# Performance work log

Hardware: AMD Instinct MI355X
Metric: run time of the kernel (lower is better)

The kernel has to match this reference:

```python
import jax, jax.numpy as jnp
import numpy as np

WS = (2, 7, 7)        # window_size (D, H, W)
DIM = 192
NHEADS = 6
NW = 64               # number of windows per image
BATCH = 32            # images -> B_ = NW*BATCH
CPB_HIDDEN = 512


def _make_buffers():
    # continuous relative coords table, shape (1, 2Wd-1, 2Wh-1, 2Ww-1, 3)
    axes = [np.arange(-(w - 1), w, dtype=np.float32) for w in WS]
    table = np.stack(np.meshgrid(*axes, indexing='ij'), axis=-1)[None]
    for i in range(3):
        table[..., i] /= (WS[i] - 1)
    table *= 8
    table = np.sign(table) * np.log2(np.abs(table) + 1.0) / np.log2(8)
    # relative position index, shape (N, N)
    coords = np.stack(np.meshgrid(np.arange(WS[0]), np.arange(WS[1]), np.arange(WS[2]), indexing='ij'))
    cf = coords.reshape(3, -1)
    rel = (cf[:, :, None] - cf[:, None, :]).transpose(1, 2, 0).astype(np.int64)
    rel[..., 0] += WS[0] - 1
    rel[..., 1] += WS[1] - 1
    rel[..., 2] += WS[2] - 1
    rel[..., 0] *= (2 * WS[1] - 1) * (2 * WS[2] - 1)
    rel[..., 1] *= 2 * WS[2] - 1
    rpi = rel.sum(-1)
    return jnp.asarray(table, jnp.float32), jnp.asarray(rpi, jnp.int32)


def setup_inputs() -> dict:
    key = jax.random.key(0)
    ks = jax.random.split(key, 10)
    N = WS[0] * WS[1] * WS[2]
    B_ = NW * BATCH
    x = jax.random.normal(ks[0], (B_, N, DIM), jnp.float32)
    mask = jax.random.normal(ks[1], (NW, N, N), jnp.float32)
    qkv_w = jax.random.normal(ks[2], (3 * DIM, DIM), jnp.float32) * 0.02
    qkv_b = jnp.zeros((3 * DIM,), jnp.float32)
    logit_scale = jnp.log(10.0 * jnp.ones((NHEADS, 1, 1), jnp.float32))
    cpb_w1 = jax.random.normal(ks[3], (CPB_HIDDEN, 3), jnp.float32) * 0.02
    cpb_b1 = jnp.zeros((CPB_HIDDEN,), jnp.float32)
    cpb_w2 = jax.random.normal(ks[4], (NHEADS, CPB_HIDDEN), jnp.float32) * 0.02
    proj_w = jax.random.normal(ks[5], (DIM, DIM), jnp.float32) * 0.02
    proj_b = jnp.zeros((DIM,), jnp.float32)
    rel_coords_table, rel_pos_index = _make_buffers()
    return dict(x=x, mask=mask, qkv_w=qkv_w, qkv_b=qkv_b, logit_scale=logit_scale,
                cpb_w1=cpb_w1, cpb_b1=cpb_b1, cpb_w2=cpb_w2,
                proj_w=proj_w, proj_b=proj_b,
                rel_coords_table=rel_coords_table, rel_pos_index=rel_pos_index)


def _l2norm(t, eps=1e-12):
    # F.normalize(dim=-1): x / max(||x||, eps)
    n = jnp.sqrt(jnp.sum(t * t, axis=-1, keepdims=True))
    return t / jnp.maximum(n, eps)


def reference(x, mask, qkv_w, qkv_b, logit_scale, cpb_w1, cpb_b1, cpb_w2,
              proj_w, proj_b, rel_coords_table, rel_pos_index):
    B_, N, C = x.shape
    H = logit_scale.shape[0]
    hd = C // H
    qkv = (x @ qkv_w.T + qkv_b).reshape(B_, N, 3, H, hd).transpose(2, 0, 3, 1, 4)
    q, k, v = qkv[0], qkv[1], qkv[2]          # (B_, H, N, hd)
    attn = jnp.einsum('bhnd,bhmd->bhnm', _l2norm(q), _l2norm(k))
    scale = jnp.exp(jnp.minimum(logit_scale, jnp.log(jnp.float32(100.0))))  # (H,1,1)
    attn = attn * scale
    # continuous position bias: MLP over coords table, gather, 16*sigmoid
    hidden = jax.nn.relu(rel_coords_table @ cpb_w1.T + cpb_b1)
    tbl = (hidden @ cpb_w2.T).reshape(-1, H)
    bias = tbl[rel_pos_index.reshape(-1)].reshape(N, N, H).transpose(2, 0, 1)
    attn = attn + (16.0 * jax.nn.sigmoid(bias))[None]
    nW = mask.shape[0]
    attn = attn.reshape(B_ // nW, nW, H, N, N) + mask[None, :, None]
    attn = jax.nn.softmax(attn.reshape(B_, H, N, N), axis=-1)
    out = jnp.einsum('bhnm,bhmd->bhnd', attn, v).transpose(0, 2, 1, 3).reshape(B_, N, C)
    return out @ proj_w.T + proj_b
```

## Files before the change

### kernel.cpp

```cpp
#include <hip/hip_runtime.h>
#include <hip/hip_bf16.h>
#include <hip/hip_fp16.h>

typedef __attribute__((ext_vector_type(8))) short short8;
typedef __attribute__((ext_vector_type(4))) float f32x4;
typedef __attribute__((ext_vector_type(4))) unsigned short us4;

#define MFMA16(a, b, c) __builtin_amdgcn_mfma_f32_16x16x32_bf16(a, b, c, 0, 0, 0)
#define LN100 4.605170185988091f

__device__ __forceinline__ short f2bf(float f) {
    unsigned u = __float_as_uint(f);
    unsigned r = (u + 0x7fffu + ((u >> 16) & 1u)) >> 16;
    return (short)r;
}
__device__ __forceinline__ float h2f(unsigned short u) {
    __half_raw r; r.x = u;
    return __half2float(__half(r));
}


__global__ __launch_bounds__(256) void k_wcvt(const float* qkv_w, const float* proj_w,
                                              short* wq, short* wp) {
    int i = blockIdx.x * 256 + threadIdx.x;
    if (i < 576 * 192) wq[i] = f2bf(qkv_w[i]);
    else {
        int j = i - 576 * 192;
        if (j < 192 * 192) wp[j] = f2bf(proj_w[j]);
    }
}

__global__ __launch_bounds__(64) void k_tbl(const float* tab, const float* w1, const float* b1,
                                            const float* w2, float* tbl) {
    int e = blockIdx.x;
    int t = threadIdx.x;
    float c0 = tab[e * 3 + 0], c1 = tab[e * 3 + 1], c2 = tab[e * 3 + 2];
    float acc[6] = {0.f, 0.f, 0.f, 0.f, 0.f, 0.f};
    for (int u = t; u < 512; u += 64) {
        float hv = c0 * w1[u * 3 + 0] + c1 * w1[u * 3 + 1] + c2 * w1[u * 3 + 2] + b1[u];
        hv = fmaxf(hv, 0.f);
        #pragma unroll
        for (int hh = 0; hh < 6; ++hh) acc[hh] += hv * w2[hh * 512 + u];
    }
    #pragma unroll
    for (int hh = 0; hh < 6; ++hh) {
        float v = acc[hh];
        for (int off = 32; off > 0; off >>= 1) v += __shfl_xor(v, off, 64);
        if (t == 0) tbl[e * 6 + hh] = v;
    }
}

__global__ __launch_bounds__(256) void k_bm(const float* tbl, const int* rpi, const float* mask,
                                            __half* bm) {
    int i = blockIdx.x * 256 + threadIdx.x;
    if (i >= 64 * 6 * 98 * 112) return;
    int k = i % 112;
    int q = (i / 112) % 98;
    int h = (i / (112 * 98)) % 6;
    int w = i / (112 * 98 * 6);
    float v;
    if (k < 98) {
        float t = tbl[rpi[q * 98 + k] * 6 + h];
        v = 16.f / (1.f + expf(-t)) + mask[(w * 98 + q) * 98 + k];
    } else v = -60000.f;
    bm[i] = __float2half(v);
}

__global__ __launch_bounds__(448) void k_fused(const float* x, const short* wq, const float* qkv_b,
                                               const float* lsc, const short* wp, const float* proj_b,
                                               const __half* bm, float* outp) {
    __shared__ short lds[79872];
    short* Qs = lds;
    short* Ks = lds + 21504;
    short* VT = lds + 43008;
    short* Bs = lds + 67584;

    const int tid = threadIdx.x;
    const int wv = tid >> 6;
    const int lane = tid & 63;
    const int l16 = lane & 15, q4 = lane >> 4;
    const int b = blockIdx.x;
    const int w = b & 63;
    const f32x4 zz = {0.f, 0.f, 0.f, 0.f};

    {
        short8 z = {0, 0, 0, 0, 0, 0, 0, 0};
        #pragma unroll
        for (int it = 0; it < 7; ++it) {
            int c = tid + it * 448;
            if (c < 3072) *(short8*)&VT[c * 8] = z;
        }
    }
    short8 af[6];
    {
        int arow = wv * 16 + l16; if (arow > 97) arow = 97;
        const float* xp = x + ((size_t)b * 98 + arow) * 192 + q4 * 8;
        #pragma unroll
        for (int ks = 0; ks < 6; ++ks) {
            float4 f0 = *(const float4*)(xp + ks * 32);
            float4 f1 = *(const float4*)(xp + ks * 32 + 4);
            union { int i4[4]; short8 s; } u;
            asm("v_cvt_pk_bf16_f32 %0, %1, %2" : "=v"(u.i4[0]) : "v"(f0.x), "v"(f0.y));
            asm("v_cvt_pk_bf16_f32 %0, %1, %2" : "=v"(u.i4[1]) : "v"(f0.z), "v"(f0.w));
            asm("v_cvt_pk_bf16_f32 %0, %1, %2" : "=v"(u.i4[2]) : "v"(f1.x), "v"(f1.y));
            asm("v_cvt_pk_bf16_f32 %0, %1, %2" : "=v"(u.i4[3]) : "v"(f1.z), "v"(f1.w));
            af[ks] = u.s;
        }
    }
    short8 s0, s1, s2, s3;
    {
        int c0 = tid, c1 = tid + 448, c2 = tid + 896, c3 = tid + 1344;
        s0 = *(const short8*)(wq + (c0 / 24) * 192 + (c0 % 24) * 8);
        s1 = *(const short8*)(wq + (c1 / 24) * 192 + (c1 % 24) * 8);
        s2 = *(const short8*)(wq + (c2 / 24) * 192 + (c2 % 24) * 8);
        if (c3 < 1536) s3 = *(const short8*)(wq + (c3 / 24) * 192 + (c3 % 24) * 8);
    }
    __syncthreads();
    {
        int c0 = tid, c1 = tid + 448, c2 = tid + 896, c3 = tid + 1344;
        *(short8*)&Bs[(c0 / 24) * 192 + (((c0 % 24) ^ ((c0 / 24) & 7)) << 3)] = s0;
        *(short8*)&Bs[(c1 / 24) * 192 + (((c1 % 24) ^ ((c1 / 24) & 7)) << 3)] = s1;
        *(short8*)&Bs[(c2 / 24) * 192 + (((c2 % 24) ^ ((c2 / 24) & 7)) << 3)] = s2;
        if (c3 < 1536) *(short8*)&Bs[(c3 / 24) * 192 + (((c3 % 24) ^ ((c3 / 24) & 7)) << 3)] = s3;
    }
    __syncthreads();

    const int row_w = wv * 16 + q4 * 4;
    #pragma unroll 1
    for (int nt = 0; nt < 9; ++nt) {
        if (nt < 8) {
            const short* wn = wq + (nt + 1) * 64 * 192;
            int c0 = tid, c1 = tid + 448, c2 = tid + 896, c3 = tid + 1344;
            s0 = *(const short8*)(wn + (c0 / 24) * 192 + (c0 % 24) * 8);
            s1 = *(const short8*)(wn + (c1 / 24) * 192 + (c1 % 24) * 8);
            s2 = *(const short8*)(wn + (c2 / 24) * 192 + (c2 % 24) * 8);
            if (c3 < 1536) s3 = *(const short8*)(wn + (c3 / 24) * 192 + (c3 % 24) * 8);
        }
        f32x4 acc[4] = {zz, zz, zz, zz};
        #pragma unroll
        for (int ks = 0; ks < 6; ++ks)
            #pragma unroll
            for (int cf = 0; cf < 4; ++cf) {
                short8 bf = *(const short8*)&Bs[(cf * 16 + l16) * 192 +
                                                (((ks * 4 + q4) ^ (l16 & 7)) << 3)];
                acc[cf] = MFMA16(af[ks], bf, acc[cf]);
            }
        #pragma unroll
        for (int p = 0; p < 2; ++p) {
            int slot = nt * 2 + p;
            int which = slot / 6;
            int h = slot - which * 6;
            float bia0 = qkv_b[slot * 32 + l16];
            float bia1 = qkv_b[slot * 32 + 16 + l16];
            float sc = 1.0f;
            if (which == 0) sc = __expf(fminf(lsc[h], LN100));
            #pragma unroll
            for (int i = 0; i < 4; ++i) {
                float v0 = acc[2 * p][i] + bia0;
                float v1 = acc[2 * p + 1][i] + bia1;
                if (which < 2) {
                    float ss = v0 * v0 + v1 * v1;
                    ss += __shfl_xor(ss, 1, 16);
                    ss += __shfl_xor(ss, 2, 16);
                    ss += __shfl_xor(ss, 4, 16);
                    ss += __shfl_xor(ss, 8, 16);
                    float rn = sc / fmaxf(sqrtf(ss), 1e-12f);
                    v0 *= rn; v1 *= rn;
                }
                int row = row_w + i;
                if (which == 2) {
                    int swz = (((row >> 3) ^ (l16 & 7)) << 3) + (row & 7);
                    VT[h * 4096 + l16 * 128 + swz]        = f2bf(v0);
                    VT[h * 4096 + (l16 + 16) * 128 + swz] = f2bf(v1);
                } else {
                    short* T = (which == 0) ? Qs : Ks;
                    int c0i = h * 32 + l16, c1i = c0i + 16;
                    T[row * 192 + (((c0i >> 3) ^ (row & 7)) << 3) + (c0i & 7)] = f2bf(v0);
                    T[row * 192 + (((c1i >> 3) ^ (row & 7)) << 3) + (c1i & 7)] = f2bf(v1);
                }
            }
        }
        __syncthreads();
        if (nt < 8) {
            int c0 = tid, c1 = tid + 448, c2 = tid + 896, c3 = tid + 1344;
            *(short8*)&Bs[(c0 / 24) * 192 + (((c0 % 24) ^ ((c0 / 24) & 7)) << 3)] = s0;
            *(short8*)&Bs[(c1 / 24) * 192 + (((c1 % 24) ^ ((c1 / 24) & 7)) << 3)] = s1;
            *(short8*)&Bs[(c2 / 24) * 192 + (((c2 % 24) ^ ((c2 / 24) & 7)) << 3)] = s2;
            if (c3 < 1536) *(short8*)&Bs[(c3 / 24) * 192 + (((c3 % 24) ^ ((c3 / 24) & 7)) << 3)] = s3;
            __syncthreads();
        }
    }

    const int rq = wv * 16 + l16;
    const int qc = rq < 98 ? rq : 97;
    const int srcA = ((q4 & 1) * 2) * 16 + l16;
    const int srcB = srcA + 16;
    const bool hi = (q4 & 2) != 0;

    #pragma unroll 1
    for (int h = 0; h < 6; ++h) {
        const __half* bmp = bm + (((size_t)w * 6 + h) * 98 + qc) * 112;
        us4 bh[7];
        #pragma unroll
        for (int ct = 0; ct < 7; ++ct) bh[ct] = *(const us4*)(bmp + ct * 16 + q4 * 4);
        short8 qf = *(const short8*)&Qs[rq * 192 + (((h * 4 + q4) ^ (l16 & 7)) << 3)];
        f32x4 cc[7];
        #pragma unroll
        for (int ct = 0; ct < 7; ++ct) {
            int rk = ct * 16 + l16;
            short8 kf = *(const short8*)&Ks[rk * 192 + (((h * 4 + q4) ^ (l16 & 7)) << 3)];
            cc[ct] = MFMA16(kf, qf, zz);
        }
        float mx = -1e30f;
        #pragma unroll
        for (int ct = 0; ct < 7; ++ct)
            #pragma unroll
            for (int i = 0; i < 4; ++i) {
                float s = cc[ct][i] + h2f(bh[ct][i]);
                cc[ct][i] = s;
                mx = fmaxf(mx, s);
            }
        mx = fmaxf(mx, __shfl_xor(mx, 16, 64));
        mx = fmaxf(mx, __shfl_xor(mx, 32, 64));
        float sm = 0.f;
        #pragma unroll
        for (int ct = 0; ct < 7; ++ct)
            #pragma unroll
            for (int i = 0; i < 4; ++i) {
                float e = __expf(cc[ct][i] - mx);
                cc[ct][i] = e;
                sm += e;
            }
        sm += __shfl_xor(sm, 16, 64);
        sm += __shfl_xor(sm, 32, 64);
        float ri = 1.f / sm;
        int W[8][2];
        W[7][0] = 0; W[7][1] = 0;
        #pragma unroll
        for (int ct = 0; ct < 7; ++ct) {
            float a0 = cc[ct][0] * ri, a1 = cc[ct][1] * ri;
            float a2 = cc[ct][2] * ri, a3 = cc[ct][3] * ri;
            asm("v_cvt_pk_bf16_f32 %0, %1, %2" : "=v"(W[ct][0]) : "v"(a0), "v"(a1));
            asm("v_cvt_pk_bf16_f32 %0, %1, %2" : "=v"(W[ct][1]) : "v"(a2), "v"(a3));
        }
        f32x4 o0 = zz, o1 = zz;
        #pragma unroll
        for (int km = 0; km < 4; ++km) {
            int A0 = __shfl(W[2 * km][0], srcA, 64), B0 = __shfl(W[2 * km + 1][0], srcA, 64);
            int A1 = __shfl(W[2 * km][1], srcA, 64), B1 = __shfl(W[2 * km + 1][1], srcA, 64);
            int A2 = __shfl(W[2 * km][0], srcB, 64), B2 = __shfl(W[2 * km + 1][0], srcB, 64);
            int A3 = __shfl(W[2 * km][1], srcB, 64), B3 = __shfl(W[2 * km + 1][1], srcB, 64);
            union { int i4[4]; short8 s; } ua;
            ua.i4[0] = hi ? B0 : A0;
            ua.i4[1] = hi ? B1 : A1;
            ua.i4[2] = hi ? B2 : A2;
            ua.i4[3] = hi ? B3 : A3;
            int sA = h * 4096 + l16 * 128 + (((km * 4 + q4) ^ (l16 & 7)) << 3);
            short8 bv0 = *(const short8*)&VT[sA];
            short8 bv1 = *(const short8*)&VT[sA + 2048];
            o0 = MFMA16(ua.s, bv0, o0);
            o1 = MFMA16(ua.s, bv1, o1);
        }
        __syncthreads();
        #pragma unroll
        for (int i = 0; i < 4; ++i) {
            int q = row_w + i;
            VT[h * 4096 + q * 32 + l16]      = f2bf(o0[i]);
            VT[h * 4096 + q * 32 + 16 + l16] = f2bf(o1[i]);
        }
    }

    {
        short8 pwst[11];
        #pragma unroll
        for (int it = 0; it < 11; ++it) {
            int c = tid + it * 448;
            if (c < 4608) pwst[it] = *(const short8*)(wp + (c / 24) * 192 + (c % 24) * 8);
        }
        #pragma unroll
        for (int it = 0; it < 11; ++it) {
            int c = tid + it * 448;
            if (c < 4608)
                *(short8*)&lds[(c / 24) * 192 + (((c % 24) ^ ((c / 24) & 7)) << 3)] = pwst[it];
        }
    }
    __syncthreads();
    {
        short8 pa[6];
        #pragma unroll
        for (int ks = 0; ks < 6; ++ks)
            pa[ks] = *(const short8*)&VT[ks * 4096 + rq * 32 + q4 * 8];
        f32x4 pacc[12] = {zz, zz, zz, zz, zz, zz, zz, zz, zz, zz, zz, zz};
        #pragma unroll
        for (int ks = 0; ks < 6; ++ks)
            #pragma unroll
            for (int cf = 0; cf < 12; ++cf) {
                short8 bf = *(const short8*)&lds[(cf * 16 + l16) * 192 +
                                                 (((ks * 4 + q4) ^ (l16 & 7)) << 3)];
                pacc[cf] = MFMA16(pa[ks], bf, pacc[cf]);
            }
        #pragma unroll
        for (int cf = 0; cf < 12; ++cf) {
            float bia = proj_b[cf * 16 + l16];
            #pragma unroll
            for (int i = 0; i < 4; ++i) {
                int q = row_w + i;
                if (q < 98)
                    outp[((size_t)b * 98 + q) * 192 + cf * 16 + l16] = pacc[cf][i] + bia;
            }
        }
    }
}

extern "C" void kernel_launch(void* const* d_in, const int* in_sizes, int n_in,
                              void* d_out, int out_size, void* d_ws, size_t ws_size,
                              hipStream_t stream) {
    const float* x    = (const float*)d_in[0];
    const float* mask = (const float*)d_in[1];
    const float* qkvw = (const float*)d_in[2];
    const float* qkvb = (const float*)d_in[3];
    const float* lsc  = (const float*)d_in[4];
    const float* w1   = (const float*)d_in[5];
    const float* b1   = (const float*)d_in[6];
    const float* w2   = (const float*)d_in[7];
    const float* pw   = (const float*)d_in[8];
    const float* pb   = (const float*)d_in[9];
    const float* tab  = (const float*)d_in[10];
    const int*   rpi  = (const int*)d_in[11];

    char* ws = (char*)d_ws;
    short*  wq  = (short*)(ws + 0);
    short*  wp  = (short*)(ws + 221184);
    float*  tbl = (float*)(ws + 294912);
    __half* bm  = (__half*)(ws + 307200);
    float*  outp = (float*)d_out;

    k_wcvt<<<576, 256, 0, stream>>>(qkvw, pw, wq, wp);
    k_tbl<<<507, 64, 0, stream>>>(tab, w1, b1, w2, tbl);
    k_bm<<<16464, 256, 0, stream>>>(tbl, rpi, mask, bm);
    k_fused<<<2048, 448, 0, stream>>>(x, wq, qkvb, lsc, wp, pb, bm, outp);
}
```

Measured before the change: 433.1 us.

## Double block size to split QKV, attention heads and projection across wave pairs

The fused kernel now launches 896 threads per block instead of 448, and pairs waves on the same 16-row group. Each wave of a pair computes half the output columns in the QKV and projection GEMMs, and three of the six heads in the attention loop. Because LDS usage limits the kernel to one block per CU, this is meant to double the resident waves per CU for better latency hiding. In exchange, the per-thread register budget under the 896-thread launch bound is halved, which risks spills in the attention phase. Each wave also reloads the same A fragments as its partner.

```diff
diff --git a/kernel.cpp b/kernel.cpp
--- a/kernel.cpp
+++ b/kernel.cpp
@@ -66,7 +66,7 @@
     bm[i] = __float2half(v);
 }
 
-__global__ __launch_bounds__(448) void k_fused(const float* x, const short* wq, const float* qkv_b,
+__global__ __launch_bounds__(896) void k_fused(const float* x, const short* wq, const float* qkv_b,
                                                const float* lsc, const short* wp, const float* proj_b,
                                                const __half* bm, float* outp) {
     __shared__ short lds[79872];
@@ -79,6 +79,8 @@
     const int wv = tid >> 6;
     const int lane = tid & 63;
     const int l16 = lane & 15, q4 = lane >> 4;
+    const int rg = wv >> 1;
+    const int hf = wv & 1;
     const int b = blockIdx.x;
     const int w = b & 63;
     const f32x4 zz = {0.f, 0.f, 0.f, 0.f};
@@ -86,14 +88,14 @@
     {
         short8 z = {0, 0, 0, 0, 0, 0, 0, 0};
         #pragma unroll
-        for (int it = 0; it < 7; ++it) {
-            int c = tid + it * 448;
+        for (int it = 0; it < 4; ++it) {
+            int c = tid + it * 896;
             if (c < 3072) *(short8*)&VT[c * 8] = z;
         }
     }
     short8 af[6];
     {
-        int arow = wv * 16 + l16; if (arow > 97) arow = 97;
+        int arow = rg * 16 + l16; if (arow > 97) arow = 97;
         const float* xp = x + ((size_t)b * 98 + arow) * 192 + q4 * 8;
         #pragma unroll
         for (int ks = 0; ks < 6; ++ks) {
@@ -107,47 +109,40 @@
             af[ks] = u.s;
         }
     }
-    short8 s0, s1, s2, s3;
-    {
-        int c0 = tid, c1 = tid + 448, c2 = tid + 896, c3 = tid + 1344;
-        s0 = *(const short8*)(wq + (c0 / 24) * 192 + (c0 % 24) * 8);
-        s1 = *(const short8*)(wq + (c1 / 24) * 192 + (c1 % 24) * 8);
-        s2 = *(const short8*)(wq + (c2 / 24) * 192 + (c2 % 24) * 8);
-        if (c3 < 1536) s3 = *(const short8*)(wq + (c3 / 24) * 192 + (c3 % 24) * 8);
+    short8 t0, t1;
+    {
+        int c1 = tid + 896;
+        t0 = *(const short8*)(wq + (tid / 24) * 192 + (tid % 24) * 8);
+        if (c1 < 1536) t1 = *(const short8*)(wq + (c1 / 24) * 192 + (c1 % 24) * 8);
     }
     __syncthreads();
     {
-        int c0 = tid, c1 = tid + 448, c2 = tid + 896, c3 = tid + 1344;
-        *(short8*)&Bs[(c0 / 24) * 192 + (((c0 % 24) ^ ((c0 / 24) & 7)) << 3)] = s0;
-        *(short8*)&Bs[(c1 / 24) * 192 + (((c1 % 24) ^ ((c1 / 24) & 7)) << 3)] = s1;
-        *(short8*)&Bs[(c2 / 24) * 192 + (((c2 % 24) ^ ((c2 / 24) & 7)) << 3)] = s2;
-        if (c3 < 1536) *(short8*)&Bs[(c3 / 24) * 192 + (((c3 % 24) ^ ((c3 / 24) & 7)) << 3)] = s3;
+        int c1 = tid + 896;
+        *(short8*)&Bs[(tid / 24) * 192 + (((tid % 24) ^ ((tid / 24) & 7)) << 3)] = t0;
+        if (c1 < 1536) *(short8*)&Bs[(c1 / 24) * 192 + (((c1 % 24) ^ ((c1 / 24) & 7)) << 3)] = t1;
     }
     __syncthreads();
 
-    const int row_w = wv * 16 + q4 * 4;
+    const int row_w = rg * 16 + q4 * 4;
     #pragma unroll 1
     for (int nt = 0; nt < 9; ++nt) {
         if (nt < 8) {
             const short* wn = wq + (nt + 1) * 64 * 192;
-            int c0 = tid, c1 = tid + 448, c2 = tid + 896, c3 = tid + 1344;
-            s0 = *(const short8*)(wn + (c0 / 24) * 192 + (c0 % 24) * 8);
-            s1 = *(const short8*)(wn + (c1 / 24) * 192 + (c1 % 24) * 8);
-            s2 = *(const short8*)(wn + (c2 / 24) * 192 + (c2 % 24) * 8);
-            if (c3 < 1536) s3 = *(const short8*)(wn + (c3 / 24) * 192 + (c3 % 24) * 8);
-        }
-        f32x4 acc[4] = {zz, zz, zz, zz};
+            int c1 = tid + 896;
+            t0 = *(const short8*)(wn + (tid / 24) * 192 + (tid % 24) * 8);
+            if (c1 < 1536) t1 = *(const short8*)(wn + (c1 / 24) * 192 + (c1 % 24) * 8);
+        }
+        f32x4 acc[2] = {zz, zz};
         #pragma unroll
         for (int ks = 0; ks < 6; ++ks)
             #pragma unroll
-            for (int cf = 0; cf < 4; ++cf) {
-                short8 bf = *(const short8*)&Bs[(cf * 16 + l16) * 192 +
+            for (int cf = 0; cf < 2; ++cf) {
+                short8 bf = *(const short8*)&Bs[((hf * 2 + cf) * 16 + l16) * 192 +
                                                 (((ks * 4 + q4) ^ (l16 & 7)) << 3)];
                 acc[cf] = MFMA16(af[ks], bf, acc[cf]);
             }
-        #pragma unroll
-        for (int p = 0; p < 2; ++p) {
-            int slot = nt * 2 + p;
+        {
+            int slot = nt * 2 + hf;
             int which = slot / 6;
             int h = slot - which * 6;
             float bia0 = qkv_b[slot * 32 + l16];
@@ -156,8 +151,8 @@
             if (which == 0) sc = __expf(fminf(lsc[h], LN100));
             #pragma unroll
             for (int i = 0; i < 4; ++i) {
-                float v0 = acc[2 * p][i] + bia0;
-                float v1 = acc[2 * p + 1][i] + bia1;
+                float v0 = acc[0][i] + bia0;
+                float v1 = acc[1][i] + bia1;
                 if (which < 2) {
                     float ss = v0 * v0 + v1 * v1;
                     ss += __shfl_xor(ss, 1, 16);
@@ -182,23 +177,22 @@
         }
         __syncthreads();
         if (nt < 8) {
-            int c0 = tid, c1 = tid + 448, c2 = tid + 896, c3 = tid + 1344;
-            *(short8*)&Bs[(c0 / 24) * 192 + (((c0 % 24) ^ ((c0 / 24) & 7)) << 3)] = s0;
-            *(short8*)&Bs[(c1 / 24) * 192 + (((c1 % 24) ^ ((c1 / 24) & 7)) << 3)] = s1;
-            *(short8*)&Bs[(c2 / 24) * 192 + (((c2 % 24) ^ ((c2 / 24) & 7)) << 3)] = s2;
-            if (c3 < 1536) *(short8*)&Bs[(c3 / 24) * 192 + (((c3 % 24) ^ ((c3 / 24) & 7)) << 3)] = s3;
+            int c1 = tid + 896;
+            *(short8*)&Bs[(tid / 24) * 192 + (((tid % 24) ^ ((tid / 24) & 7)) << 3)] = t0;
+            if (c1 < 1536) *(short8*)&Bs[(c1 / 24) * 192 + (((c1 % 24) ^ ((c1 / 24) & 7)) << 3)] = t1;
             __syncthreads();
         }
     }
 
-    const int rq = wv * 16 + l16;
+    const int rq = rg * 16 + l16;
     const int qc = rq < 98 ? rq : 97;
     const int srcA = ((q4 & 1) * 2) * 16 + l16;
     const int srcB = srcA + 16;
     const bool hi = (q4 & 2) != 0;
 
     #pragma unroll 1
-    for (int h = 0; h < 6; ++h) {
+    for (int j = 0; j < 3; ++j) {
+        const int h = hf * 3 + j;
         const __half* bmp = bm + (((size_t)w * 6 + h) * 98 + qc) * 112;
         us4 bh[7];
         #pragma unroll
@@ -271,15 +265,15 @@
     }
 
     {
-        short8 pwst[11];
-        #pragma unroll
-        for (int it = 0; it < 11; ++it) {
-            int c = tid + it * 448;
+        short8 pwst[6];
+        #pragma unroll
+        for (int it = 0; it < 6; ++it) {
+            int c = tid + it * 896;
             if (c < 4608) pwst[it] = *(const short8*)(wp + (c / 24) * 192 + (c % 24) * 8);
         }
         #pragma unroll
-        for (int it = 0; it < 11; ++it) {
-            int c = tid + it * 448;
+        for (int it = 0; it < 6; ++it) {
+            int c = tid + it * 896;
             if (c < 4608)
                 *(short8*)&lds[(c / 24) * 192 + (((c % 24) ^ ((c / 24) & 7)) << 3)] = pwst[it];
         }
@@ -290,23 +284,24 @@
         #pragma unroll
         for (int ks = 0; ks < 6; ++ks)
             pa[ks] = *(const short8*)&VT[ks * 4096 + rq * 32 + q4 * 8];
-        f32x4 pacc[12] = {zz, zz, zz, zz, zz, zz, zz, zz, zz, zz, zz, zz};
+        f32x4 pacc[6] = {zz, zz, zz, zz, zz, zz};
         #pragma unroll
         for (int ks = 0; ks < 6; ++ks)
             #pragma unroll
-            for (int cf = 0; cf < 12; ++cf) {
-                short8 bf = *(const short8*)&lds[(cf * 16 + l16) * 192 +
+            for (int cf = 0; cf < 6; ++cf) {
+                short8 bf = *(const short8*)&lds[((hf * 6 + cf) * 16 + l16) * 192 +
                                                  (((ks * 4 + q4) ^ (l16 & 7)) << 3)];
                 pacc[cf] = MFMA16(pa[ks], bf, pacc[cf]);
             }
         #pragma unroll
-        for (int cf = 0; cf < 12; ++cf) {
-            float bia = proj_b[cf * 16 + l16];
+        for (int cf = 0; cf < 6; ++cf) {
+            int cg = (hf * 6 + cf) * 16 + l16;
+            float bia = proj_b[cg];
             #pragma unroll
             for (int i = 0; i < 4; ++i) {
                 int q = row_w + i;
                 if (q < 98)
-                    outp[((size_t)b * 98 + q) * 192 + cf * 16 + l16] = pacc[cf][i] + bia;
+                    outp[((size_t)b * 98 + q) * 192 + cg] = pacc[cf][i] + bia;
             }
         }
     }
@@ -338,5 +333,5 @@
     k_wcvt<<<576, 256, 0, stream>>>(qkvw, pw, wq, wp);
     k_tbl<<<507, 64, 0, stream>>>(tab, w1, b1, w2, tbl);
     k_bm<<<16464, 256, 0, stream>>>(tbl, rpi, mask, bm);
-    k_fused<<<2048, 448, 0, stream>>>(x, wq, qkvb, lsc, wp, pb, bm, outp);
-}
+    k_fused<<<2048, 896, 0, stream>>>(x, wq, qkvb, lsc, wp, pb, bm, outp);
+}
```

Measured after the change: 377.2 us (median of 2 runs). 12.9% less time.
